# Kernel tuning notes

Hardware: AMD Instinct MI355X
Metric: run time of the kernel (lower is better)

Reference implementation:

```python
import jax, jax.numpy as jnp
import numpy as np

# YOLOv2 anchors (grid units), 5 anchors, anchor_step=2
ANCHORS = np.array([[1.3221, 1.73145], [3.19275, 4.00944], [5.05587, 8.09892],
                    [9.47112, 4.84053], [11.2364, 10.0071]], dtype=np.float32)
NUM_CLASSES = 2
NOOBJECT_SCALE = 1.0
OBJECT_SCALE = 5.0
COORD_SCALE = 1.0
CLASS_SCALE = 1.0
SIL_THRESH = 0.6
T = 50  # max targets per image


def iou_cwh(b1, b2):
    # boxes (..., 4) as (cx, cy, w, h); broadcasting IoU, faithful to bbox_iou(x1y1x2y2=False)
    x1, y1, w1, h1 = b1[..., 0], b1[..., 1], b1[..., 2], b1[..., 3]
    x2, y2, w2, h2 = b2[..., 0], b2[..., 1], b2[..., 2], b2[..., 3]
    uw = jnp.maximum(x1 + w1 * 0.5, x2 + w2 * 0.5) - jnp.minimum(x1 - w1 * 0.5, x2 - w2 * 0.5)
    uh = jnp.maximum(y1 + h1 * 0.5, y2 + h2 * 0.5) - jnp.minimum(y1 - h1 * 0.5, y2 - h2 * 0.5)
    cw = w1 + w2 - uw
    ch = h1 + h2 - uh
    carea = jnp.where((cw <= 0) | (ch <= 0), 0.0, cw * ch)
    return carea / (w1 * h1 + w2 * h2 - carea)


def yolo_v2_loss(output, target):
    anchors = jnp.asarray(ANCHORS)
    nA, nC = anchors.shape[0], NUM_CLASSES
    nB, _, nH, nW = output.shape
    out5 = output.reshape(nB, nA, 5 + nC + 1, nH, nW)
    aw, ah = anchors[:, 0], anchors[:, 1]

    # ---------- detached predicted boxes (torch used .data) ----------
    po = jax.lax.stop_gradient(out5)
    gx_grid = jnp.arange(nW, dtype=output.dtype)
    gy_grid = jnp.arange(nH, dtype=output.dtype)
    px = jax.nn.sigmoid(po[:, :, 0]) + gx_grid[None, None, None, :]
    py = jax.nn.sigmoid(po[:, :, 1]) + gy_grid[None, None, :, None]
    pw = jnp.exp(po[:, :, 2]) * aw[None, :, None, None]
    ph = jnp.exp(po[:, :, 3]) * ah[None, :, None, None]
    pred = jnp.stack([px, py, pw, ph], -1).reshape(nB, nA * nH * nW, 4)  # (nB, nP, 4)

    # ---------- parse targets ----------
    tgt = target.reshape(nB, T, 6)  # (cls, x, y, w, h, lr)
    tcls_v = tgt[..., 0]
    gx = tgt[..., 1] * nW
    gy = tgt[..., 2] * nH
    gw = tgt[..., 3] * nW
    gh = tgt[..., 4] * nH
    lr_v = tgt[..., 5]
    # torch breaks at first x==0; emulate with cumulative validity
    valid = jnp.cumprod((tgt[..., 1] != 0).astype(jnp.int32), axis=1).astype(bool)

    # ---------- silence mask: max IoU of every pred box vs all gt ----------
    gt = jnp.stack([gx, gy, gw, gh], -1)  # (nB, T, 4)
    ious = iou_cwh(pred[:, :, None, :], gt[:, None, :, :])  # (nB, nP, T)
    cur_ious = jnp.where(valid[:, None, :], ious, 0.0).max(-1)  # (nB, nP)
    conf_mask0 = jnp.where(cur_ious > SIL_THRESH, 0.0, NOOBJECT_SCALE).reshape(-1)

    # ---------- best anchor per gt (centered IoU, argmax == first strict max) ----------
    z = jnp.zeros_like(gw)
    gt0 = jnp.stack([z, z, gw, gh], -1)[:, :, None, :]  # (nB, T, 1, 4)
    za = jnp.zeros_like(aw)
    an0 = jnp.stack([za, za, aw, ah], -1)[None, None, :, :]  # (1, 1, nA, 4)
    best_n = jnp.argmax(iou_cwh(an0, gt0), axis=-1)  # (nB, T)

    gi = gx.astype(jnp.int32)
    gj = gy.astype(jnp.int32)
    aw_b = aw[best_n]
    ah_b = ah[best_n]
    tx_v = gx - gi
    ty_v = gy - gj
    tw_v = jnp.log(gw / aw_b)
    th_v = jnp.log(gh / ah_b)
    idx_in_b = best_n * (nH * nW) + gj * nW + gi  # (nB, T)
    pred_at = jnp.take_along_axis(pred, idx_in_b[:, :, None], axis=1)  # (nB, T, 4)
    tconf_v = iou_cwh(gt, pred_at)  # (nB, T)

    Ntot = nB * nA * nH * nW
    flat_idx = jnp.where(valid, jnp.arange(nB)[:, None] * (nA * nH * nW) + idx_in_b, Ntot)
    one = jnp.ones_like(tx_v)
    # rows: coord_mask, cls_mask, conf_mask, tx, ty, tw, th, tconf, tcls, lr_mask, tconf_lr
    vals = jnp.stack([one, one, OBJECT_SCALE * one, tx_v, ty_v, tw_v, th_v,
                      tconf_v, tcls_v, one, lr_v], 0)  # (11, nB, T)
    state0 = jnp.zeros((11, Ntot), output.dtype).at[2].set(conf_mask0)

    def body(st, inp):
        i, v = inp
        return st.at[:, i].set(v, mode='drop'), None

    state, _ = jax.lax.scan(body, state0, (flat_idx.T, jnp.transpose(vals, (2, 0, 1))))
    state = jax.lax.stop_gradient(state)
    shp = (nB, nA, nH, nW)
    (coord_mask, cls_mask, conf_mask, tx, ty, tw, th,
     tconf, tcls, lr_mask, tconf_lr) = [state[i].reshape(shp) for i in range(11)]

    # ---------- differentiable predictions ----------
    x = jax.nn.sigmoid(out5[:, :, 0])
    y = jax.nn.sigmoid(out5[:, :, 1])
    w = out5[:, :, 2]
    h = out5[:, :, 3]
    conf = jax.nn.sigmoid(out5[:, :, 4])
    conf_lr = jax.nn.sigmoid(out5[:, :, 5 + nC])
    # torch: view(nB*nA, nC, nH*nW).transpose(1,2) -> row order (b, a, h, w)
    cls_logits = jnp.transpose(out5[:, :, 5:5 + nC], (0, 1, 3, 4, 2)).reshape(-1, nC)

    def mse_half(a, b, m):
        return 0.5 * jnp.sum((a * m - b * m) ** 2)

    loss_x = COORD_SCALE * mse_half(x, tx, coord_mask)
    loss_y = COORD_SCALE * mse_half(y, ty, coord_mask)
    loss_w = COORD_SCALE * mse_half(w, tw, coord_mask)
    loss_h = COORD_SCALE * mse_half(h, th, coord_mask)
    loss_conf = mse_half(conf, tconf, jnp.sqrt(conf_mask))
    logp = jax.nn.log_softmax(cls_logits, axis=-1)
    tcls_flat = tcls.reshape(-1).astype(jnp.int32)
    ce = -jnp.take_along_axis(logp, tcls_flat[:, None], axis=1)[:, 0]
    loss_cls = CLASS_SCALE * jnp.sum(ce * cls_mask.reshape(-1))
    loss_conf_lr = mse_half(conf_lr, tconf_lr, lr_mask)
    loss = loss_x + loss_y + loss_w + loss_h + loss_conf + loss_cls + 0.5 * loss_conf_lr
    return loss / nB


def setup_inputs() -> dict:
    key = jax.random.key(0)
    k1, k2, k3, k4, k5 = jax.random.split(key, 5)
    nB, nH, nW = 16, 96, 96
    nA, nC = 5, 2
    output = jax.random.normal(k1, (nB, nA * (5 + nC + 1), nH, nW), jnp.float32) * 0.5
    # targets: (cls, x, y, w, h, lr) per slot, all 50 slots valid (x != 0)
    cls = jax.random.randint(k2, (nB, T, 1), 0, nC).astype(jnp.float32)
    xy = jax.random.uniform(k3, (nB, T, 2), minval=0.05, maxval=0.95)
    wh = jax.random.uniform(k4, (nB, T, 2), minval=0.05, maxval=0.5)
    lr = jax.random.uniform(k5, (nB, T, 1))
    target = jnp.concatenate([cls, xy, wh, lr], axis=-1).reshape(nB, T * 6)
    return {"output": output, "target": target}


def reference(output, target):
    return yolo_v2_loss(output, target)
```

## Files before the change

### kernel.cpp

```cpp
#include <hip/hip_runtime.h>
#include <math.h>

#define NB 16
#define NA 5
#define NH 96
#define NW 96
#define TT 50
#define HW (NH*NW)
#define APB (NA*HW)
#define CPT 4

__device__ __constant__ float c_aw[NA] = {1.3221f, 3.19275f, 5.05587f, 9.47112f, 11.2364f};
__device__ __constant__ float c_ah[NA] = {1.73145f, 4.00944f, 8.09892f, 4.84053f, 10.0071f};

__device__ __forceinline__ float sigmoidf(float x) { return 1.0f / (1.0f + __expf(-x)); }

__global__ void prep_kernel(const float* __restrict__ target,
                            float* __restrict__ gth,
                            float* __restrict__ gtc,
                            int* __restrict__ map) {
    int b = blockIdx.x;
    int t = threadIdx.x;
    __shared__ int s_cell[TT], s_valid[TT];

    float xraw = (t < TT) ? target[(b*TT + t)*6 + 1] : 1.0f;
    unsigned long long m = __ballot(xraw != 0.0f);

    int valid = 0, best = 0, cell = -1, gi = 0, gj = 0;
    float gx=0, gy=0, gw=1, gh=1, tcls=0, lr=0;
    if (t < TT) {
        valid = (((~m) & ((2ull << t) - 1ull)) == 0ull) ? 1 : 0;
        const float* tg = target + (b*TT + t)*6;
        tcls = tg[0];
        gx = tg[1]*NW; gy = tg[2]*NH; gw = tg[3]*NW; gh = tg[4]*NH;
        lr = tg[5];
        float bestiou = -1.0f;
        for (int a = 0; a < NA; ++a) {
            float inter = fminf(gw, c_aw[a]) * fminf(gh, c_ah[a]);
            float iou = inter / (gw*gh + c_aw[a]*c_ah[a] - inter);
            if (iou > bestiou) { bestiou = iou; best = a; }
        }
        gi = (int)gx; gj = (int)gy;
        cell = best*HW + gj*NW + gi;
        s_cell[t]  = valid ? cell : -1;
        s_valid[t] = valid;
    }
    __syncthreads();
    if (t < TT) {
        float* rh = gth + (b*TT + t)*8;
        if (valid) {
            rh[0] = gx - 0.5f*gw; rh[1] = gx + 0.5f*gw;
            rh[2] = gy - 0.5f*gh; rh[3] = gy + 0.5f*gh;
            rh[4] = -0.6f*gw*gh;
        } else {
            rh[0] = 0.0f; rh[1] = 0.0f; rh[2] = 0.0f; rh[3] = 0.0f;
            rh[4] = -1e30f;
        }
        rh[5] = 0.0f; rh[6] = 0.0f; rh[7] = 0.0f;
        float* rc = gtc + (b*TT + t)*8;
        rc[0] = gw*gh;
        rc[1] = gx - (float)gi;  rc[2] = gy - (float)gj;
        rc[3] = logf(gw / c_aw[best]); rc[4] = logf(gh / c_ah[best]);
        rc[5] = tcls; rc[6] = lr; rc[7] = 0.0f;
        if (valid) {
            int winner = 1;
            for (int u = t + 1; u < TT; ++u)
                if (s_valid[u] && s_cell[u] == cell) { winner = 0; break; }
            if (winner) map[b*APB + cell] = t;
        }
    }
}

__global__ __launch_bounds__(256)
void loss_kernel(const float* __restrict__ outp,
                 const float* __restrict__ gth,
                 const float* __restrict__ gtc,
                 const int* __restrict__ map,
                 float* __restrict__ loss) {
    __shared__ float4 sgt4[TT*2];
    float* sgt = (float*)sgt4;
    int b   = blockIdx.y;
    int tid = threadIdx.x;
    if (tid < TT*2) sgt4[tid] = ((const float4*)(gth + b*TT*8))[tid];
    __syncthreads();

    int q     = blockIdx.x*256 + tid;
    int cell0 = q*CPT;
    int a   = cell0 / HW;
    int rem = cell0 - a*HW;
    int j   = rem / NW;
    int i0  = rem - j*NW;

    const float* base = outp + (size_t)((b*NA + a)*8)*HW + rem;
    float4 v0 = *(const float4*)(base + 0*HW);
    float4 v1 = *(const float4*)(base + 1*HW);
    float4 v2 = *(const float4*)(base + 2*HW);
    float4 v3 = *(const float4*)(base + 3*HW);
    float4 v4 = *(const float4*)(base + 4*HW);
    float o0[CPT] = {v0.x, v0.y, v0.z, v0.w};
    float o1[CPT] = {v1.x, v1.y, v1.z, v1.w};
    float o2[CPT] = {v2.x, v2.y, v2.z, v2.w};
    float o3[CPT] = {v3.x, v3.y, v3.z, v3.w};
    float o4[CPT] = {v4.x, v4.y, v4.z, v4.w};

    float aw = c_aw[a], ah = c_ah[a];
    float pxl[CPT], pxr[CPT], pyl[CPT], pyr[CPT], parea[CPT], maxv[CPT];
    #pragma unroll
    for (int c = 0; c < CPT; ++c) {
        float sx = sigmoidf(o0[c]), sy = sigmoidf(o1[c]);
        float px = sx + (float)(i0 + c);
        float py = sy + (float)j;
        float pw = __expf(o2[c]) * aw;
        float ph = __expf(o3[c]) * ah;
        pxl[c] = px - 0.5f*pw; pxr[c] = px + 0.5f*pw;
        pyl[c] = py - 0.5f*ph; pyr[c] = py + 0.5f*ph;
        parea[c] = pw*ph;
        maxv[c] = -1e30f;
    }

    #pragma unroll 10
    for (int t = 0; t < TT; ++t) {
        float4 ra  = *(const float4*)(sgt + t*8);
        float g06n = sgt[t*8 + 4];
        #pragma unroll
        for (int c = 0; c < CPT; ++c) {
            float cw = fminf(pxr[c], ra.y) - fmaxf(pxl[c], ra.x);
            float ch = fminf(pyr[c], ra.w) - fmaxf(pyl[c], ra.z);
            float carea = fmaxf(cw, 0.0f) * fmaxf(ch, 0.0f);
            maxv[c] = fmaxf(maxv[c], fmaf(1.6f, carea, g06n));
        }
    }

    int4 mp = *(const int4*)(map + b*APB + cell0);
    int mc[CPT] = {mp.x, mp.y, mp.z, mp.w};

    float acc = 0.0f;
    #pragma unroll
    for (int c = 0; c < CPT; ++c) {
        float conf = sigmoidf(o4[c]);
        int tw_idx = mc[c];
        if (tw_idx >= 0) {
            const float* cr = gtc + (b*TT + tw_idx)*8;
            float garea = cr[0], tx = cr[1], ty = cr[2];
            float tw = cr[3], th = cr[4], tcls = cr[5], lr = cr[6];
            float gxl = sgt[tw_idx*8+0], gxr = sgt[tw_idx*8+1];
            float gyl = sgt[tw_idx*8+2], gyr = sgt[tw_idx*8+3];
            float cw = fminf(pxr[c], gxr) - fmaxf(pxl[c], gxl);
            float ch = fminf(pyr[c], gyr) - fmaxf(pyl[c], gyl);
            float carea = fmaxf(cw, 0.0f) * fmaxf(ch, 0.0f);
            float tconf = carea / (parea[c] + garea - carea);
            float dc = conf - tconf;
            float term = 2.5f*dc*dc;
            float sx = sigmoidf(o0[c]), sy = sigmoidf(o1[c]);
            float dx = sx - tx, dy = sy - ty, dw = o2[c] - tw, dh = o3[c] - th;
            term += 0.5f*(dx*dx + dy*dy + dw*dw + dh*dh);
            float o5 = base[5*HW + c], o6 = base[6*HW + c], o7 = base[7*HW + c];
            float mm  = fmaxf(o5, o6);
            float lse = mm + __logf(__expf(o5 - mm) + __expf(o6 - mm));
            term += lse - ((tcls != 0.0f) ? o6 : o5);
            float dl = sigmoidf(o7) - lr;
            term += 0.25f*dl*dl;
            acc += term;
        } else {
            acc += (maxv[c] > 0.6f*parea[c]) ? 0.0f : 0.5f*conf*conf;
        }
    }

    for (int off = 32; off > 0; off >>= 1) acc += __shfl_down(acc, off, 64);
    __shared__ float ssum[4];
    int lane = tid & 63, wid = tid >> 6;
    if (lane == 0) ssum[wid] = acc;
    __syncthreads();
    if (tid == 0) {
        float s = (ssum[0] + ssum[1]) + (ssum[2] + ssum[3]);
        atomicAdd(loss, s * (1.0f/NB));
    }
}

extern "C" void kernel_launch(void* const* d_in, const int* in_sizes, int n_in,
                              void* d_out, int out_size, void* d_ws, size_t ws_size,
                              hipStream_t stream) {
    const float* output = (const float*)d_in[0];
    const float* target = (const float*)d_in[1];
    float* gth = (float*)d_ws;
    float* gtc = gth + NB*TT*8;
    int*   map = (int*)((char*)d_ws + 65536);
    float* out = (float*)d_out;

    hipMemsetAsync(out, 0, (size_t)out_size*sizeof(float), stream);
    hipMemsetAsync(map, 0xFF, (size_t)NB*APB*sizeof(int), stream);
    hipLaunchKernelGGL(prep_kernel, dim3(NB), dim3(64), 0, stream,
                       target, gth, gtc, map);
    dim3 grid(APB/(256*CPT), NB);
    hipLaunchKernelGGL(loss_kernel, grid, dim3(256), 0, stream,
                       output, gth, gtc, map, out);
}
```

Before: 94.92 us.

## Fuse target prep into loss kernel and build per-block cell map in shared memory

Merges the separate target-preparation kernel into the loss kernel. Each block recomputes the per-image ground-truth boxes in shared memory and builds a local cell-to-target map for its own 1024 cells. This removes the 2.9 MB map memset, one kernel launch, and the global round trips for gth/gtc/map. In exchange, every block redundantly parses the 50 targets, which adds a small prologue and an extra barrier per block.

```diff
diff --git a/kernel.cpp b/kernel.cpp
--- a/kernel.cpp
+++ b/kernel.cpp
@@ -9,83 +9,79 @@
 #define HW (NH*NW)
 #define APB (NA*HW)
 #define CPT 4
+#define CPB (256*CPT)
 
 __device__ __constant__ float c_aw[NA] = {1.3221f, 3.19275f, 5.05587f, 9.47112f, 11.2364f};
 __device__ __constant__ float c_ah[NA] = {1.73145f, 4.00944f, 8.09892f, 4.84053f, 10.0071f};
 
 __device__ __forceinline__ float sigmoidf(float x) { return 1.0f / (1.0f + __expf(-x)); }
 
-__global__ void prep_kernel(const float* __restrict__ target,
-                            float* __restrict__ gth,
-                            float* __restrict__ gtc,
-                            int* __restrict__ map) {
-    int b = blockIdx.x;
-    int t = threadIdx.x;
-    __shared__ int s_cell[TT], s_valid[TT];
+__global__ __launch_bounds__(256)
+void yolo_loss_fused(const float* __restrict__ outp,
+                     const float* __restrict__ target,
+                     float* __restrict__ loss) {
+    __shared__ float s_hot[TT*8];
+    __shared__ float s_cold[TT*8];
+    __shared__ int   s_cell[TT];
+    __shared__ int   s_map[CPB];
+    __shared__ float s_sum[4];
 
-    float xraw = (t < TT) ? target[(b*TT + t)*6 + 1] : 1.0f;
-    unsigned long long m = __ballot(xraw != 0.0f);
+    int b   = blockIdx.y;
+    int tid = threadIdx.x;
+    int base_cell = blockIdx.x * CPB;
 
-    int valid = 0, best = 0, cell = -1, gi = 0, gj = 0;
-    float gx=0, gy=0, gw=1, gh=1, tcls=0, lr=0;
-    if (t < TT) {
-        valid = (((~m) & ((2ull << t) - 1ull)) == 0ull) ? 1 : 0;
-        const float* tg = target + (b*TT + t)*6;
-        tcls = tg[0];
-        gx = tg[1]*NW; gy = tg[2]*NH; gw = tg[3]*NW; gh = tg[4]*NH;
-        lr = tg[5];
-        float bestiou = -1.0f;
-        for (int a = 0; a < NA; ++a) {
-            float inter = fminf(gw, c_aw[a]) * fminf(gh, c_ah[a]);
-            float iou = inter / (gw*gh + c_aw[a]*c_ah[a] - inter);
-            if (iou > bestiou) { bestiou = iou; best = a; }
+    #pragma unroll
+    for (int k = 0; k < CPT; ++k) s_map[tid + k*256] = -1;
+
+    if (tid < 64) {
+        int t = tid;
+        float xraw = (t < TT) ? target[(b*TT + t)*6 + 1] : 1.0f;
+        unsigned long long m = __ballot(xraw != 0.0f);
+        if (t < TT) {
+            int valid = (((~m) & ((2ull << t) - 1ull)) == 0ull) ? 1 : 0;
+            const float* tg = target + (b*TT + t)*6;
+            float tcls = tg[0];
+            float gx = tg[1]*NW, gy = tg[2]*NH, gw = tg[3]*NW, gh = tg[4]*NH;
+            float lr = tg[5];
+            int best = 0; float bi = -1.0f;
+            for (int a2 = 0; a2 < NA; ++a2) {
+                float inter = fminf(gw, c_aw[a2]) * fminf(gh, c_ah[a2]);
+                float iou = inter / (gw*gh + c_aw[a2]*c_ah[a2] - inter);
+                if (iou > bi) { bi = iou; best = a2; }
+            }
+            int gi = (int)gx, gj = (int)gy;
+            s_cell[t] = valid ? (best*HW + gj*NW + gi) : -1;
+            float* rh = &s_hot[t*8];
+            if (valid) {
+                rh[0] = gx - 0.5f*gw; rh[1] = gx + 0.5f*gw;
+                rh[2] = gy - 0.5f*gh; rh[3] = gy + 0.5f*gh;
+                rh[4] = -0.6f*gw*gh;
+            } else {
+                rh[0] = 0.0f; rh[1] = 0.0f; rh[2] = 0.0f; rh[3] = 0.0f;
+                rh[4] = -1e30f;
+            }
+            rh[5] = 0.0f; rh[6] = 0.0f; rh[7] = 0.0f;
+            float* rc = &s_cold[t*8];
+            rc[0] = gw*gh;
+            rc[1] = gx - (float)gi;  rc[2] = gy - (float)gj;
+            rc[3] = logf(gw / c_aw[best]); rc[4] = logf(gh / c_ah[best]);
+            rc[5] = tcls; rc[6] = lr; rc[7] = 0.0f;
         }
-        gi = (int)gx; gj = (int)gy;
-        cell = best*HW + gj*NW + gi;
-        s_cell[t]  = valid ? cell : -1;
-        s_valid[t] = valid;
     }
     __syncthreads();
-    if (t < TT) {
-        float* rh = gth + (b*TT + t)*8;
-        if (valid) {
-            rh[0] = gx - 0.5f*gw; rh[1] = gx + 0.5f*gw;
-            rh[2] = gy - 0.5f*gh; rh[3] = gy + 0.5f*gh;
-            rh[4] = -0.6f*gw*gh;
-        } else {
-            rh[0] = 0.0f; rh[1] = 0.0f; rh[2] = 0.0f; rh[3] = 0.0f;
-            rh[4] = -1e30f;
-        }
-        rh[5] = 0.0f; rh[6] = 0.0f; rh[7] = 0.0f;
-        float* rc = gtc + (b*TT + t)*8;
-        rc[0] = gw*gh;
-        rc[1] = gx - (float)gi;  rc[2] = gy - (float)gj;
-        rc[3] = logf(gw / c_aw[best]); rc[4] = logf(gh / c_ah[best]);
-        rc[5] = tcls; rc[6] = lr; rc[7] = 0.0f;
-        if (valid) {
+    if (tid < TT) {
+        int cell = s_cell[tid];
+        if (cell >= 0) {
             int winner = 1;
-            for (int u = t + 1; u < TT; ++u)
-                if (s_valid[u] && s_cell[u] == cell) { winner = 0; break; }
-            if (winner) map[b*APB + cell] = t;
+            for (int u = tid + 1; u < TT; ++u)
+                if (s_cell[u] == cell) { winner = 0; break; }
+            int local = cell - base_cell;
+            if (winner && (unsigned)local < CPB) s_map[local] = tid;
         }
     }
-}
-
-__global__ __launch_bounds__(256)
-void loss_kernel(const float* __restrict__ outp,
-                 const float* __restrict__ gth,
-                 const float* __restrict__ gtc,
-                 const int* __restrict__ map,
-                 float* __restrict__ loss) {
-    __shared__ float4 sgt4[TT*2];
-    float* sgt = (float*)sgt4;
-    int b   = blockIdx.y;
-    int tid = threadIdx.x;
-    if (tid < TT*2) sgt4[tid] = ((const float4*)(gth + b*TT*8))[tid];
     __syncthreads();
 
-    int q     = blockIdx.x*256 + tid;
-    int cell0 = q*CPT;
+    int cell0 = base_cell + tid*CPT;
     int a   = cell0 / HW;
     int rem = cell0 - a*HW;
     int j   = rem / NW;
@@ -97,11 +93,13 @@
     float4 v2 = *(const float4*)(base + 2*HW);
     float4 v3 = *(const float4*)(base + 3*HW);
     float4 v4 = *(const float4*)(base + 4*HW);
+    int4  mp  = *(const int4*)(&s_map[tid*CPT]);
     float o0[CPT] = {v0.x, v0.y, v0.z, v0.w};
     float o1[CPT] = {v1.x, v1.y, v1.z, v1.w};
     float o2[CPT] = {v2.x, v2.y, v2.z, v2.w};
     float o3[CPT] = {v3.x, v3.y, v3.z, v3.w};
     float o4[CPT] = {v4.x, v4.y, v4.z, v4.w};
+    int   mc[CPT] = {mp.x, mp.y, mp.z, mp.w};
 
     float aw = c_aw[a], ah = c_ah[a];
     float pxl[CPT], pxr[CPT], pyl[CPT], pyr[CPT], parea[CPT], maxv[CPT];
@@ -120,8 +118,8 @@
 
     #pragma unroll 10
     for (int t = 0; t < TT; ++t) {
-        float4 ra  = *(const float4*)(sgt + t*8);
-        float g06n = sgt[t*8 + 4];
+        float4 ra  = *(const float4*)(&s_hot[t*8]);
+        float g06n = s_hot[t*8 + 4];
         #pragma unroll
         for (int c = 0; c < CPT; ++c) {
             float cw = fminf(pxr[c], ra.y) - fmaxf(pxl[c], ra.x);
@@ -131,22 +129,18 @@
         }
     }
 
-    int4 mp = *(const int4*)(map + b*APB + cell0);
-    int mc[CPT] = {mp.x, mp.y, mp.z, mp.w};
-
     float acc = 0.0f;
     #pragma unroll
     for (int c = 0; c < CPT; ++c) {
         float conf = sigmoidf(o4[c]);
         int tw_idx = mc[c];
         if (tw_idx >= 0) {
-            const float* cr = gtc + (b*TT + tw_idx)*8;
+            const float* cr = &s_cold[tw_idx*8];
             float garea = cr[0], tx = cr[1], ty = cr[2];
             float tw = cr[3], th = cr[4], tcls = cr[5], lr = cr[6];
-            float gxl = sgt[tw_idx*8+0], gxr = sgt[tw_idx*8+1];
-            float gyl = sgt[tw_idx*8+2], gyr = sgt[tw_idx*8+3];
-            float cw = fminf(pxr[c], gxr) - fmaxf(pxl[c], gxl);
-            float ch = fminf(pyr[c], gyr) - fmaxf(pyl[c], gyl);
+            const float* rh = &s_hot[tw_idx*8];
+            float cw = fminf(pxr[c], rh[1]) - fmaxf(pxl[c], rh[0]);
+            float ch = fminf(pyr[c], rh[3]) - fmaxf(pyl[c], rh[2]);
             float carea = fmaxf(cw, 0.0f) * fmaxf(ch, 0.0f);
             float tconf = carea / (parea[c] + garea - carea);
             float dc = conf - tconf;
@@ -167,12 +161,11 @@
     }
 
     for (int off = 32; off > 0; off >>= 1) acc += __shfl_down(acc, off, 64);
-    __shared__ float ssum[4];
     int lane = tid & 63, wid = tid >> 6;
-    if (lane == 0) ssum[wid] = acc;
+    if (lane == 0) s_sum[wid] = acc;
     __syncthreads();
     if (tid == 0) {
-        float s = (ssum[0] + ssum[1]) + (ssum[2] + ssum[3]);
+        float s = (s_sum[0] + s_sum[1]) + (s_sum[2] + s_sum[3]);
         atomicAdd(loss, s * (1.0f/NB));
     }
 }
@@ -182,16 +175,10 @@
                               hipStream_t stream) {
     const float* output = (const float*)d_in[0];
     const float* target = (const float*)d_in[1];
-    float* gth = (float*)d_ws;
-    float* gtc = gth + NB*TT*8;
-    int*   map = (int*)((char*)d_ws + 65536);
     float* out = (float*)d_out;
 
     hipMemsetAsync(out, 0, (size_t)out_size*sizeof(float), stream);
-    hipMemsetAsync(map, 0xFF, (size_t)NB*APB*sizeof(int), stream);
-    hipLaunchKernelGGL(prep_kernel, dim3(NB), dim3(64), 0, stream,
-                       target, gth, gtc, map);
-    dim3 grid(APB/(256*CPT), NB);
-    hipLaunchKernelGGL(loss_kernel, grid, dim3(256), 0, stream,
-                       output, gth, gtc, map, out);
+    dim3 grid(APB/CPB, NB);
+    hipLaunchKernelGGL(yolo_loss_fused, grid, dim3(256), 0, stream,
+                       output, target, out);
 }
```

Measured after the change: 86.28 us. 1.1x faster.
